# Performance work log

Hardware: AMD Instinct MI355X
Metric: run time of the kernel (lower is better)

## Reference

```python
import jax, jax.numpy as jnp
import numpy as np

NEG_SLOPE = 0.2


def _gat_layer(x, W, a_src, a_dst, b, src, dst, heads, out_dim, concat):
    # x: [N, F_in]; W: [F_in, heads*out_dim]; a_src/a_dst: [heads, out_dim]
    N = x.shape[0]
    h = (x @ W).reshape(N, heads, out_dim)              # [N, H, D]
    alpha_src = jnp.sum(h * a_src[None], axis=-1)       # [N, H]
    alpha_dst = jnp.sum(h * a_dst[None], axis=-1)       # [N, H]
    e = jax.nn.leaky_relu(alpha_src[src] + alpha_dst[dst], NEG_SLOPE)  # [E, H]
    # scatter-softmax over incoming edges of each destination node
    e_max = jax.ops.segment_max(e, dst, num_segments=N)            # [N, H]
    e_exp = jnp.exp(e - e_max[dst])                                 # [E, H]
    e_sum = jax.ops.segment_sum(e_exp, dst, num_segments=N)        # [N, H]
    alpha = e_exp / e_sum[dst]                                      # [E, H]
    # weighted scatter-sum of source features
    msg = alpha[:, :, None] * h[src]                                # [E, H, D]
    out = jax.ops.segment_sum(msg, dst, num_segments=N)             # [N, H, D]
    if concat:
        out = out.reshape(N, heads * out_dim)
    else:
        out = out.mean(axis=1)
    return out + b


def setup_inputs() -> dict:
    key = jax.random.key(0)
    ks = jax.random.split(key, 9)
    N, E, F_in, C = 100000, 1600000, 512, 40
    x = jax.random.normal(ks[0], (N, F_in), dtype=jnp.float32)
    edge_index = jax.random.randint(ks[1], (2, E), 0, N, dtype=jnp.int64)
    s = 0.05
    return {
        "x": x,
        "edge_index": edge_index,
        "W1": jax.random.normal(ks[2], (F_in, 64), dtype=jnp.float32) * s,
        "att_src1": jax.random.normal(ks[3], (8, 8), dtype=jnp.float32) * s,
        "att_dst1": jax.random.normal(ks[4], (8, 8), dtype=jnp.float32) * s,
        "b1": jnp.zeros((64,), dtype=jnp.float32),
        "W2": jax.random.normal(ks[5], (64, C), dtype=jnp.float32) * s,
        "att_src2": jax.random.normal(ks[6], (1, C), dtype=jnp.float32) * s,
        "att_dst2": jax.random.normal(ks[7], (1, C), dtype=jnp.float32) * s,
        "b2": jnp.zeros((C,), dtype=jnp.float32),
    }


def reference(x, edge_index, W1, att_src1, att_dst1, b1, W2, att_src2, att_dst2, b2):
    N = x.shape[0]
    # PyG GATConv default add_self_loops=True
    loops = jnp.tile(jnp.arange(N, dtype=edge_index.dtype)[None, :], (2, 1))
    ei = jnp.concatenate([edge_index, loops], axis=1)
    src, dst = ei[0], ei[1]
    # dropout layers are identity at inference
    h = _gat_layer(x, W1, att_src1, att_dst1, b1, src, dst, heads=8, out_dim=8, concat=True)
    h = jax.nn.elu(h)
    out = _gat_layer(h, W2, att_src2, att_dst2, b2, src, dst, heads=1, out_dim=40, concat=True)
    return jax.nn.log_softmax(out, axis=1)
```

## Files before the change

### kernel.cpp

```cpp
#include <hip/hip_runtime.h>
#include <hip/hip_bf16.h>

typedef __bf16 bf16x8 __attribute__((ext_vector_type(8)));
typedef float f32x4 __attribute__((ext_vector_type(4)));
typedef unsigned u32x2 __attribute__((ext_vector_type(2)));
typedef unsigned u32x4 __attribute__((ext_vector_type(4)));

#define LR_SLOPE 0.2f
#define NBKMAX 256
#define BCAP   12288

static __device__ __forceinline__ unsigned short f2bf(float f){
  union { float f; unsigned u; } v; v.f = f;
  unsigned u = v.u;
  u += 0x7fffu + ((u >> 16) & 1u);
  return (unsigned short)(u >> 16);
}
static __device__ __forceinline__ float bf2f(unsigned short us){
  union { unsigned u; float f; } v; v.u = ((unsigned)us) << 16;
  return v.f;
}
static __device__ __forceinline__ unsigned pk2(float a, float b){
  return (unsigned)f2bf(a) | ((unsigned)f2bf(b) << 16);
}
static __device__ __forceinline__ unsigned char f2e4m3(float f){
  return (unsigned char)(__builtin_amdgcn_cvt_pk_fp8_f32(f, 0.f, 0, false) & 0xff);
}
static __device__ __forceinline__ float e4m32f(unsigned b){
  return __builtin_amdgcn_cvt_f32_fp8(b, 0);
}
typedef float f32x4v __attribute__((ext_vector_type(4)));
static __device__ __forceinline__ f32x4v ntl4(const float* p){
  return __builtin_nontemporal_load((const f32x4v*)p);
}

__global__ void prep_w_kernel(const float* __restrict__ W1, const float* __restrict__ W2,
                              unsigned short* __restrict__ wt1, unsigned short* __restrict__ wt2,
                              int* __restrict__ bcnt){
  int t = blockIdx.x*256 + threadIdx.x;
  if (t < 512*64){
    int k = t >> 6, n = t & 63;
    wt1[n*512 + k] = f2bf(W1[t]);
  } else if (t < 512*64 + 48*64){
    int t2 = t - 512*64;
    int c = t2 >> 6, k = t2 & 63;
    wt2[t2] = (c < 40) ? f2bf(W2[k*40 + c]) : (unsigned short)0;
  } else {
    int t3 = t - (512*64 + 48*64);
    if (t3 < NBKMAX) bcnt[t3] = 0;
  }
}

__global__ __launch_bounds__(256) void gemm1_kernel(
    const float* __restrict__ x, const unsigned short* __restrict__ wt1,
    const float* __restrict__ aw_s, const float* __restrict__ aw_d,
    unsigned char* __restrict__ h1p,
    unsigned short* __restrict__ as1p, float* __restrict__ ad1, int N)
{
  __shared__ unsigned short Alds[64*72];
  const int tid = threadIdx.x;
  const int wv = tid >> 6, lane = tid & 63;
  const int c0 = lane & 15, g = lane >> 4;
  const int rowbase = blockIdx.x * 64;

  const int sr = tid >> 2, sq = tid & 3;
  const int grow = rowbase + sr;
  const bool rv = grow < N;
  const float* xp = x + (size_t)grow*512 + sq*16;
  unsigned short* wls = Alds + sr*72 + sq*16;

  f32x4 acc[4];
  acc[0] = acc[1] = acc[2] = acc[3] = (f32x4){0.f,0.f,0.f,0.f};

  const unsigned short* bp0 = wt1 + (size_t)(wv*16 + c0)*512 + g*8;

  for (int kt = 0; kt < 8; ++kt){
    f32x4v f0 = {0,0,0,0}, f1 = {0,0,0,0}, f2 = {0,0,0,0}, f3 = {0,0,0,0};
    if (rv){
      const float* p = xp + kt*64;
      f0 = ntl4(p); f1 = ntl4(p+4); f2 = ntl4(p+8); f3 = ntl4(p+12);
    }
    u32x4 w0 = { pk2(f0.x,f0.y), pk2(f0.z,f0.w), pk2(f1.x,f1.y), pk2(f1.z,f1.w) };
    u32x4 w1 = { pk2(f2.x,f2.y), pk2(f2.z,f2.w), pk2(f3.x,f3.y), pk2(f3.z,f3.w) };
    if (kt) __syncthreads();
    *(u32x4*)wls       = w0;
    *(u32x4*)(wls + 8) = w1;
    __syncthreads();
    bf16x8 b0 = *(const bf16x8*)(bp0 + kt*64);
    bf16x8 b1 = *(const bf16x8*)(bp0 + kt*64 + 32);
    #pragma unroll
    for (int mi = 0; mi < 4; ++mi){
      const unsigned short* ap = Alds + (mi*16 + c0)*72 + g*8;
      bf16x8 a0 = *(const bf16x8*)ap;
      bf16x8 a1 = *(const bf16x8*)(ap + 32);
      acc[mi] = __builtin_amdgcn_mfma_f32_16x16x32_bf16(a0, b0, acc[mi], 0,0,0);
      acc[mi] = __builtin_amdgcn_mfma_f32_16x16x32_bf16(a1, b1, acc[mi], 0,0,0);
    }
  }
  const int hh = wv*2 + (c0 >> 3);
  const float aws_l = aw_s[hh*8 + (c0 & 7)];
  const float awd_l = aw_d[hh*8 + (c0 & 7)];
  #pragma unroll
  for (int mi = 0; mi < 4; ++mi){
    #pragma unroll
    for (int i = 0; i < 4; ++i){
      int row = rowbase + mi*16 + 4*g + i;
      float av = acc[mi][i];
      if (row < N) h1p[(size_t)row*64 + wv*16 + c0] = f2e4m3(av);
      float ss = av * aws_l;
      float dd = av * awd_l;
      ss += __shfl_xor(ss, 1); ss += __shfl_xor(ss, 2); ss += __shfl_xor(ss, 4);
      dd += __shfl_xor(dd, 1); dd += __shfl_xor(dd, 2); dd += __shfl_xor(dd, 4);
      if (row < N && (c0 & 7) == 0){
        as1p[row*8 + hh] = f2bf(ss);
        ad1[row*8 + hh]  = dd;
      }
    }
  }
}

__global__ __launch_bounds__(256) void bucketA_kernel(
    const int* __restrict__ ei, int* __restrict__ bcnt,
    unsigned* __restrict__ bucketed, int E, int M, int NBK)
{
  __shared__ int hist[NBKMAX];
  __shared__ int gb[NBKMAX];
  const int tid = threadIdx.x;
  const int t0 = blockIdx.x * 2048;
  for (int i = tid; i < NBK; i += 256) hist[i] = 0;
  __syncthreads();

  unsigned pe[8]; int bk[8], rnk[8];
  #pragma unroll
  for (int j = 0; j < 8; ++j){
    int m = t0 + j*256 + tid;
    if (m < M){
      int s, d;
      if (m < E){ s = ei[m]; d = ei[E + m]; }
      else      { s = d = m - E; }
      bk[j] = d >> 9;
      pe[j] = ((unsigned)s << 9) | (unsigned)(d & 511);
      rnk[j] = atomicAdd(&hist[bk[j]], 1);
    } else bk[j] = -1;
  }
  __syncthreads();
  for (int i = tid; i < NBK; i += 256) gb[i] = atomicAdd(&bcnt[i], hist[i]);
  __syncthreads();
  #pragma unroll
  for (int j = 0; j < 8; ++j){
    if (bk[j] >= 0) bucketed[(size_t)bk[j]*BCAP + gb[bk[j]] + rnk[j]] = pe[j];
  }
}

__global__ void scanB_kernel(const int* __restrict__ bcnt, int* __restrict__ bstart,
                             int* __restrict__ rowstart, int NBK, int N, int M){
  __shared__ int sc[256];
  int t = threadIdx.x;
  int v = (t < NBK) ? bcnt[t] : 0;
  sc[t] = v; __syncthreads();
  for (int off = 1; off < 256; off <<= 1){
    int u = (t >= off) ? sc[t-off] : 0;
    __syncthreads();
    sc[t] += u;
    __syncthreads();
  }
  if (t < NBK) bstart[t] = sc[t] - v;
  if (t == 0) rowstart[N] = M;
}

__global__ __launch_bounds__(512) void bucketB_kernel(
    const unsigned* __restrict__ bucketed, const int* __restrict__ bcnt,
    const int* __restrict__ bstart,
    int* __restrict__ rowstart, int* __restrict__ csr, int N)
{
  __shared__ int cnt[512];
  __shared__ int cur[512];
  const int k = blockIdx.x;
  const int nodebase = k << 9;
  const int nn = min(512, N - nodebase);
  const int t = threadIdx.x;
  cnt[t] = 0;
  __syncthreads();
  const int ck = bcnt[k];
  const unsigned* bp = bucketed + (size_t)k*BCAP;
  for (int m = t; m < ck; m += 512) atomicAdd(&cnt[bp[m] & 511], 1);
  __syncthreads();
  int myc = cnt[t];
  cur[t] = myc; __syncthreads();
  for (int off = 1; off < 512; off <<= 1){
    int u = (t >= off) ? cur[t-off] : 0;
    __syncthreads();
    cur[t] += u;
    __syncthreads();
  }
  const int base = bstart[k];
  int excl = base + cur[t] - myc;
  if (t < nn) rowstart[nodebase + t] = excl;
  cnt[t] = excl;
  __syncthreads();
  for (int m = t; m < ck; m += 512){
    unsigned e = bp[m];
    int pos = atomicAdd(&cnt[e & 511], 1);
    csr[pos] = (int)(e >> 9);
  }
}

__global__ __launch_bounds__(256) void l1agg_kernel(
    const int* __restrict__ rowstart, const int* __restrict__ csr,
    const unsigned short* __restrict__ as1p,
    const float* __restrict__ ad1,
    const unsigned char* __restrict__ h1p,
    const float* __restrict__ b1,
    unsigned short* __restrict__ g1b, int N)
{
  int wid = blockIdx.x*4 + (threadIdx.x >> 6);
  if (wid >= N) return;
  const int lane = threadIdx.x & 63;
  const int jq  = lane >> 3;
  const int hq  = lane & 7;
  const int par = lane >> 4;
  const int q   = lane & 15;
  const int hh  = q >> 1;
  int r0 = rowstart[wid], r1 = rowstart[wid+1];
  int cnt = r1 - r0;
  int cap = cnt < 64 ? cnt : 64;
  int myidx = csr[r0 + (lane < cap ? lane : cap-1)];
  const float advq = ad1[wid*8 + hq];

  float a0 = 0.f, a1 = 0.f, a2 = 0.f, a3 = 0.f, den = 0.f;
  for (int c = 0; c < cap; c += 8){
    int se = __shfl(myidx, c + jq);
    float t = bf2f(as1p[se*8 + hq]) + advq;
    t = (t > 0.f) ? t : LR_SLOPE*t;
    float w = __expf(t);
    if (c + jq >= cap) w = 0.f;
    den += w;
    #pragma unroll
    for (int j = 0; j < 2; ++j){
      int s8 = 4*j + par;
      int sj = __shfl(myidx, c + s8);
      float wj = __shfl(w, s8*8 + hh);
      unsigned hv = *(const unsigned*)(h1p + (size_t)sj*64 + 4*q);
      a0 = fmaf(wj, __builtin_amdgcn_cvt_f32_fp8(hv, 0), a0);
      a1 = fmaf(wj, __builtin_amdgcn_cvt_f32_fp8(hv, 1), a1);
      a2 = fmaf(wj, __builtin_amdgcn_cvt_f32_fp8(hv, 2), a2);
      a3 = fmaf(wj, __builtin_amdgcn_cvt_f32_fp8(hv, 3), a3);
    }
  }
  for (int r = r0 + 64; r < r1; ++r){
    int sx = csr[r];
    float t = bf2f(as1p[sx*8 + hq]) + advq;
    t = (t > 0.f) ? t : LR_SLOPE*t;
    float w = __expf(t);
    if (lane < 8) den += w;
    float wj = __shfl(w, hh);
    if (par == 0){
      unsigned hv = *(const unsigned*)(h1p + (size_t)sx*64 + 4*q);
      a0 = fmaf(wj, __builtin_amdgcn_cvt_f32_fp8(hv, 0), a0);
      a1 = fmaf(wj, __builtin_amdgcn_cvt_f32_fp8(hv, 1), a1);
      a2 = fmaf(wj, __builtin_amdgcn_cvt_f32_fp8(hv, 2), a2);
      a3 = fmaf(wj, __builtin_amdgcn_cvt_f32_fp8(hv, 3), a3);
    }
  }
  den += __shfl_xor(den, 8); den += __shfl_xor(den, 16); den += __shfl_xor(den, 32);
  a0 += __shfl_xor(a0, 16); a0 += __shfl_xor(a0, 32);
  a1 += __shfl_xor(a1, 16); a1 += __shfl_xor(a1, 32);
  a2 += __shfl_xor(a2, 16); a2 += __shfl_xor(a2, 32);
  a3 += __shfl_xor(a3, 16); a3 += __shfl_xor(a3, 32);
  if (lane < 16){
    float rdv = 1.f / __shfl(den, hh);
    float v0 = fmaf(a0, rdv, b1[4*q]);
    float v1 = fmaf(a1, rdv, b1[4*q + 1]);
    float v2 = fmaf(a2, rdv, b1[4*q + 2]);
    float v3 = fmaf(a3, rdv, b1[4*q + 3]);
    v0 = (v0 > 0.f) ? v0 : (__expf(v0) - 1.f);
    v1 = (v1 > 0.f) ? v1 : (__expf(v1) - 1.f);
    v2 = (v2 > 0.f) ? v2 : (__expf(v2) - 1.f);
    v3 = (v3 > 0.f) ? v3 : (__expf(v3) - 1.f);
    u32x2 pk = { pk2(v0, v1), pk2(v2, v3) };
    *(u32x2*)(g1b + (size_t)wid*64 + 4*q) = pk;
  }
}

__global__ __launch_bounds__(256) void gemm2_kernel(
    const unsigned short* __restrict__ g1b, const unsigned short* __restrict__ wt2,
    const float* __restrict__ aw_s, const float* __restrict__ aw_d,
    unsigned char* __restrict__ h2p, float* __restrict__ as2, float* __restrict__ ad2, int N)
{
  __shared__ unsigned short Alds[64*72];
  const int tid = threadIdx.x;
  const int wv = tid >> 6, lane = tid & 63;
  const int c0 = lane & 15, g = lane >> 4;
  const int rowbase = blockIdx.x * 64;

  const int sr = tid >> 2, sq = tid & 3;
  const int grow = rowbase + sr;
  const bool rv = grow < N;
  u32x4 w0 = {0,0,0,0}, w1 = {0,0,0,0};
  if (rv){
    const u32x4* gp = (const u32x4*)(g1b + (size_t)grow*64 + sq*16);
    w0 = gp[0];
    w1 = gp[1];
  }
  unsigned short* wls = Alds + sr*72 + sq*16;
  *(u32x4*)wls       = w0;
  *(u32x4*)(wls + 8) = w1;
  __syncthreads();

  f32x4 acc[3];
  acc[0] = acc[1] = acc[2] = (f32x4){0.f,0.f,0.f,0.f};
  #pragma unroll
  for (int t2 = 0; t2 < 2; ++t2){
    const unsigned short* ap = Alds + (wv*16 + c0)*72 + t2*32 + g*8;
    bf16x8 a = *(const bf16x8*)ap;
    #pragma unroll
    for (int nf = 0; nf < 3; ++nf){
      bf16x8 b = *(const bf16x8*)(wt2 + (nf*16 + c0)*64 + t2*32 + g*8);
      acc[nf] = __builtin_amdgcn_mfma_f32_16x16x32_bf16(a, b, acc[nf], 0,0,0);
    }
  }
  float aws[3], awd[3];
  aws[0] = aw_s[c0];      awd[0] = aw_d[c0];
  aws[1] = aw_s[16 + c0]; awd[1] = aw_d[16 + c0];
  aws[2] = (c0 < 8) ? aw_s[32 + c0] : 0.f;
  awd[2] = (c0 < 8) ? aw_d[32 + c0] : 0.f;
  #pragma unroll
  for (int i = 0; i < 4; ++i){
    int row = rowbase + wv*16 + 4*g + i;
    float ss = 0.f, dd = 0.f;
    #pragma unroll
    for (int nf = 0; nf < 3; ++nf){
      int col = nf*16 + c0;
      float av = acc[nf][i];
      if (row < N && col < 40) h2p[(size_t)row*40 + col] = f2e4m3(av);
      float m = (col < 40) ? av : 0.f;
      ss = fmaf(m, aws[nf], ss);
      dd = fmaf(m, awd[nf], dd);
    }
    ss += __shfl_xor(ss, 1); ss += __shfl_xor(ss, 2);
    ss += __shfl_xor(ss, 4); ss += __shfl_xor(ss, 8);
    dd += __shfl_xor(dd, 1); dd += __shfl_xor(dd, 2);
    dd += __shfl_xor(dd, 4); dd += __shfl_xor(dd, 8);
    if (row < N && c0 == 0){ as2[row] = ss; ad2[row] = dd; }
  }
}

__global__ __launch_bounds__(256) void l2agg_kernel(
    const int* __restrict__ rowstart, const int* __restrict__ csr,
    const float* __restrict__ as2, const float* __restrict__ ad2,
    const unsigned char* __restrict__ h2p, const float* __restrict__ b2,
    float* __restrict__ out, int N)
{
  int wid = blockIdx.x*4 + (threadIdx.x >> 6);
  if (wid >= N) return;
  const int lane = threadIdx.x & 63;
  const int eg = lane / 10;
  const int ql = lane - eg*10;
  const bool gl = lane < 60;
  int r0 = rowstart[wid], r1 = rowstart[wid+1];
  int cnt = r1 - r0;
  int cap = cnt < 64 ? cnt : 64;
  int myidx = csr[r0 + (lane < cap ? lane : cap-1)];
  const float adv = ad2[wid];

  float t = as2[myidx] + adv;
  t = (t > 0.f) ? t : LR_SLOPE*t;
  float w = __expf(t);
  if (lane >= cap) w = 0.f;
  float den = w;
  #pragma unroll
  for (int off = 32; off; off >>= 1) den += __shfl_xor(den, off);

  float a0 = 0.f, a1 = 0.f, a2 = 0.f, a3 = 0.f;
  for (int c = 0; c < cap; c += 6){
    int slot = c + eg;
    int slc  = slot < 63 ? slot : 63;
    float wj = __shfl(w, slc);
    if (slot >= cap || !gl) wj = 0.f;
    int sj = __shfl(myidx, slc);
    if (gl){
      unsigned hv = *(const unsigned*)(h2p + (size_t)sj*40 + 4*ql);
      a0 = fmaf(wj, __builtin_amdgcn_cvt_f32_fp8(hv, 0), a0);
      a1 = fmaf(wj, __builtin_amdgcn_cvt_f32_fp8(hv, 1), a1);
      a2 = fmaf(wj, __builtin_amdgcn_cvt_f32_fp8(hv, 2), a2);
      a3 = fmaf(wj, __builtin_amdgcn_cvt_f32_fp8(hv, 3), a3);
    }
  }
  for (int r = r0 + 64; r < r1; ++r){
    int sx = csr[r];
    float tt = as2[sx] + adv;
    tt = (tt > 0.f) ? tt : LR_SLOPE*tt;
    float ww = __expf(tt);
    den += ww;
    if (eg == 0){
      unsigned hv = *(const unsigned*)(h2p + (size_t)sx*40 + 4*ql);
      a0 = fmaf(ww, __builtin_amdgcn_cvt_f32_fp8(hv, 0), a0);
      a1 = fmaf(ww, __builtin_amdgcn_cvt_f32_fp8(hv, 1), a1);
      a2 = fmaf(ww, __builtin_amdgcn_cvt_f32_fp8(hv, 2), a2);
      a3 = fmaf(ww, __builtin_amdgcn_cvt_f32_fp8(hv, 3), a3);
    }
  }
  float t0 = a0, t1 = a1, t2 = a2, t3 = a3;
  #pragma unroll
  for (int gix = 1; gix < 6; ++gix){
    int src = ((eg + gix) % 6)*10 + ql;
    t0 += __shfl(a0, src);
    t1 += __shfl(a1, src);
    t2 += __shfl(a2, src);
    t3 += __shfl(a3, src);
  }
  float rdv = 1.f/den;
  float v0 = gl ? fmaf(t0, rdv, b2[4*ql])     : -1e30f;
  float v1 = gl ? fmaf(t1, rdv, b2[4*ql + 1]) : -1e30f;
  float v2 = gl ? fmaf(t2, rdv, b2[4*ql + 2]) : -1e30f;
  float v3 = gl ? fmaf(t3, rdv, b2[4*ql + 3]) : -1e30f;
  float m = fmaxf(fmaxf(v0, v1), fmaxf(v2, v3));
  #pragma unroll
  for (int off = 32; off; off >>= 1) m = fmaxf(m, __shfl_xor(m, off));
  float sum = (eg == 0) ? (__expf(v0-m) + __expf(v1-m) + __expf(v2-m) + __expf(v3-m)) : 0.f;
  #pragma unroll
  for (int off = 32; off; off >>= 1) sum += __shfl_xor(sum, off);
  if (eg == 0){
    float ls = m + __logf(sum);
    f32x4 o = { v0 - ls, v1 - ls, v2 - ls, v3 - ls };
    *(f32x4*)(out + (size_t)wid*40 + 4*ql) = o;
  }
}

extern "C" void kernel_launch(void* const* d_in, const int* in_sizes, int n_in,
                              void* d_out, int out_size, void* d_ws, size_t ws_size,
                              hipStream_t stream)
{
  const float* x   = (const float*)d_in[0];
  const int*   ei  = (const int*)d_in[1];
  const float* W1  = (const float*)d_in[2];
  const float* aS1 = (const float*)d_in[3];
  const float* aD1 = (const float*)d_in[4];
  const float* b1  = (const float*)d_in[5];
  const float* W2  = (const float*)d_in[6];
  const float* aS2 = (const float*)d_in[7];
  const float* aD2 = (const float*)d_in[8];
  const float* b2  = (const float*)d_in[9];

  const int N   = in_sizes[0] / 512;
  const int E   = in_sizes[1] / 2;
  const int M   = E + N;
  const int NBK = (N + 511) >> 9;

  char* base = (char*)d_ws;
  size_t off = 0;
  auto alloc = [&](size_t bytes)->char* {
    char* p = base + off;
    off += (bytes + 255) & ~(size_t)255;
    return p;
  };
  unsigned char*  h1p  = (unsigned char*)alloc((size_t)N*64);
  unsigned short* g1b  = (unsigned short*)alloc((size_t)N*64*2);
  unsigned short* as1p = (unsigned short*)alloc((size_t)N*8*2);
  float* ad1      = (float*)alloc((size_t)N*8*4);
  int*   rowstart = (int*)alloc((size_t)(N+1)*4);
  int*   bcnt     = (int*)alloc((size_t)NBKMAX*4);
  int*   bstart   = (int*)alloc((size_t)NBKMAX*4);
  int*   csr      = (int*)alloc((size_t)M*4);
  unsigned* bucketed = (unsigned*)alloc((size_t)NBKMAX*BCAP*4);
  unsigned short* wt1 = (unsigned short*)alloc(64*512*2);
  unsigned short* wt2 = (unsigned short*)alloc(48*64*2);
  unsigned char* h2p = h1p;
  float* as2 = (float*)as1p;
  float* ad2 = (float*)ad1;
  float* outp = (float*)d_out;

  prep_w_kernel<<<141, 256, 0, stream>>>(W1, W2, wt1, wt2, bcnt);
  gemm1_kernel<<<(N+63)/64, 256, 0, stream>>>(x, wt1, aS1, aD1, h1p, as1p, ad1, N);
  bucketA_kernel<<<(M+2047)/2048, 256, 0, stream>>>(ei, bcnt, bucketed, E, M, NBK);
  scanB_kernel<<<1, 256, 0, stream>>>(bcnt, bstart, rowstart, NBK, N, M);
  bucketB_kernel<<<NBK, 512, 0, stream>>>(bucketed, bcnt, bstart, rowstart, csr, N);
  l1agg_kernel<<<(N+3)/4, 256, 0, stream>>>(rowstart, csr, as1p, ad1, h1p, b1, g1b, N);
  gemm2_kernel<<<(N+63)/64, 256, 0, stream>>>(g1b, wt2, aS2, aD2, h2p, as2, ad2, N);
  l2agg_kernel<<<(N+3)/4, 256, 0, stream>>>(rowstart, csr, as2, ad2, h2p, b2, outp, N);
}
```

Before: 253.5 us.

## Pack layer-2 source logit with fp8 features and fuse bucket scan

New measurement: 253.4 us. Within noise of the previous version (-0.0%).

```diff
diff --git a/kernel.cpp b/kernel.cpp
--- a/kernel.cpp
+++ b/kernel.cpp
@@ -152,35 +152,30 @@
   }
 }
 
-__global__ void scanB_kernel(const int* __restrict__ bcnt, int* __restrict__ bstart,
-                             int* __restrict__ rowstart, int NBK, int N, int M){
-  __shared__ int sc[256];
-  int t = threadIdx.x;
-  int v = (t < NBK) ? bcnt[t] : 0;
-  sc[t] = v; __syncthreads();
-  for (int off = 1; off < 256; off <<= 1){
-    int u = (t >= off) ? sc[t-off] : 0;
-    __syncthreads();
-    sc[t] += u;
-    __syncthreads();
-  }
-  if (t < NBK) bstart[t] = sc[t] - v;
-  if (t == 0) rowstart[N] = M;
-}
-
 __global__ __launch_bounds__(512) void bucketB_kernel(
     const unsigned* __restrict__ bucketed, const int* __restrict__ bcnt,
-    const int* __restrict__ bstart,
-    int* __restrict__ rowstart, int* __restrict__ csr, int N)
+    int* __restrict__ rowstart, int* __restrict__ csr, int N, int M, int NBK)
 {
   __shared__ int cnt[512];
   __shared__ int cur[512];
+  __shared__ int basevar;
   const int k = blockIdx.x;
   const int nodebase = k << 9;
   const int nn = min(512, N - nodebase);
   const int t = threadIdx.x;
+
+  cur[t] = (t < NBK) ? bcnt[t] : 0;
+  __syncthreads();
+  for (int off = 1; off < 256; off <<= 1){
+    int u = (t >= off && t < 256) ? cur[t-off] : 0;
+    __syncthreads();
+    if (t < 256) cur[t] += u;
+    __syncthreads();
+  }
+  if (t == 0) basevar = (k > 0) ? cur[k-1] : 0;
   cnt[t] = 0;
   __syncthreads();
+
   const int ck = bcnt[k];
   const unsigned* bp = bucketed + (size_t)k*BCAP;
   for (int m = t; m < ck; m += 512) atomicAdd(&cnt[bp[m] & 511], 1);
@@ -193,9 +188,10 @@
     cur[t] += u;
     __syncthreads();
   }
-  const int base = bstart[k];
+  const int base = basevar;
   int excl = base + cur[t] - myc;
   if (t < nn) rowstart[nodebase + t] = excl;
+  if (k == 0 && t == 0) rowstart[N] = M;
   cnt[t] = excl;
   __syncthreads();
   for (int m = t; m < ck; m += 512){
@@ -285,7 +281,7 @@
 __global__ __launch_bounds__(256) void gemm2_kernel(
     const unsigned short* __restrict__ g1b, const unsigned short* __restrict__ wt2,
     const float* __restrict__ aw_s, const float* __restrict__ aw_d,
-    unsigned char* __restrict__ h2p, float* __restrict__ as2, float* __restrict__ ad2, int N)
+    unsigned char* __restrict__ h2x, float* __restrict__ ad2, int N)
 {
   __shared__ unsigned short Alds[64*72];
   const int tid = threadIdx.x;
@@ -332,7 +328,7 @@
     for (int nf = 0; nf < 3; ++nf){
       int col = nf*16 + c0;
       float av = acc[nf][i];
-      if (row < N && col < 40) h2p[(size_t)row*40 + col] = f2e4m3(av);
+      if (row < N && col < 40) h2x[(size_t)row*64 + 4 + col] = f2e4m3(av);
       float m = (col < 40) ? av : 0.f;
       ss = fmaf(m, aws[nf], ss);
       dd = fmaf(m, awd[nf], dd);
@@ -341,89 +337,92 @@
     ss += __shfl_xor(ss, 4); ss += __shfl_xor(ss, 8);
     dd += __shfl_xor(dd, 1); dd += __shfl_xor(dd, 2);
     dd += __shfl_xor(dd, 4); dd += __shfl_xor(dd, 8);
-    if (row < N && c0 == 0){ as2[row] = ss; ad2[row] = dd; }
+    if (row < N && c0 == 0){
+      *(float*)(h2x + (size_t)row*64) = ss;
+      ad2[row] = dd;
+    }
   }
 }
 
 __global__ __launch_bounds__(256) void l2agg_kernel(
     const int* __restrict__ rowstart, const int* __restrict__ csr,
-    const float* __restrict__ as2, const float* __restrict__ ad2,
-    const unsigned char* __restrict__ h2p, const float* __restrict__ b2,
-    float* __restrict__ out, int N)
+    const unsigned char* __restrict__ h2x, const float* __restrict__ ad2,
+    const float* __restrict__ b2, float* __restrict__ out, int N)
 {
   int wid = blockIdx.x*4 + (threadIdx.x >> 6);
   if (wid >= N) return;
   const int lane = threadIdx.x & 63;
-  const int eg = lane / 10;
-  const int ql = lane - eg*10;
-  const bool gl = lane < 60;
+  const int eg = lane / 11;
+  const int il = lane - eg*11;
+  const bool valid = eg < 5;
   int r0 = rowstart[wid], r1 = rowstart[wid+1];
   int cnt = r1 - r0;
   int cap = cnt < 64 ? cnt : 64;
   int myidx = csr[r0 + (lane < cap ? lane : cap-1)];
   const float adv = ad2[wid];
 
-  float t = as2[myidx] + adv;
-  t = (t > 0.f) ? t : LR_SLOPE*t;
-  float w = __expf(t);
-  if (lane >= cap) w = 0.f;
-  float den = w;
-  #pragma unroll
-  for (int off = 32; off; off >>= 1) den += __shfl_xor(den, off);
-
-  float a0 = 0.f, a1 = 0.f, a2 = 0.f, a3 = 0.f;
-  for (int c = 0; c < cap; c += 6){
+  float a0 = 0.f, a1 = 0.f, a2 = 0.f, a3 = 0.f, den = 0.f;
+  for (int c = 0; c < cap; c += 5){
     int slot = c + eg;
-    int slc  = slot < 63 ? slot : 63;
-    float wj = __shfl(w, slc);
-    if (slot >= cap || !gl) wj = 0.f;
+    int slc  = slot < cap ? slot : cap-1;
     int sj = __shfl(myidx, slc);
-    if (gl){
-      unsigned hv = *(const unsigned*)(h2p + (size_t)sj*40 + 4*ql);
+    unsigned hv = valid ? *(const unsigned*)(h2x + (size_t)sj*64 + 4*il) : 0u;
+    union { unsigned u; float f; } cv; cv.u = hv;
+    float t = cv.f + adv;
+    t = (t > 0.f) ? t : LR_SLOPE*t;
+    float w = __expf(t);
+    if (slot >= cap || !valid) w = 0.f;
+    if (il == 0) den += w;
+    float wj = __shfl(w, eg*11);
+    a0 = fmaf(wj, __builtin_amdgcn_cvt_f32_fp8(hv, 0), a0);
+    a1 = fmaf(wj, __builtin_amdgcn_cvt_f32_fp8(hv, 1), a1);
+    a2 = fmaf(wj, __builtin_amdgcn_cvt_f32_fp8(hv, 2), a2);
+    a3 = fmaf(wj, __builtin_amdgcn_cvt_f32_fp8(hv, 3), a3);
+  }
+  for (int r = r0 + 64; r < r1; ++r){
+    int sx = csr[r];
+    unsigned hv = valid ? *(const unsigned*)(h2x + (size_t)sx*64 + 4*il) : 0u;
+    union { unsigned u; float f; } cv; cv.u = hv;
+    float t = cv.f + adv;
+    t = (t > 0.f) ? t : LR_SLOPE*t;
+    float w = __expf(t);
+    float wj = __shfl(w, 0);
+    if (lane == 0) den += wj;
+    if (eg == 0){
       a0 = fmaf(wj, __builtin_amdgcn_cvt_f32_fp8(hv, 0), a0);
       a1 = fmaf(wj, __builtin_amdgcn_cvt_f32_fp8(hv, 1), a1);
       a2 = fmaf(wj, __builtin_amdgcn_cvt_f32_fp8(hv, 2), a2);
       a3 = fmaf(wj, __builtin_amdgcn_cvt_f32_fp8(hv, 3), a3);
     }
   }
-  for (int r = r0 + 64; r < r1; ++r){
-    int sx = csr[r];
-    float tt = as2[sx] + adv;
-    tt = (tt > 0.f) ? tt : LR_SLOPE*tt;
-    float ww = __expf(tt);
-    den += ww;
-    if (eg == 0){
-      unsigned hv = *(const unsigned*)(h2p + (size_t)sx*40 + 4*ql);
-      a0 = fmaf(ww, __builtin_amdgcn_cvt_f32_fp8(hv, 0), a0);
-      a1 = fmaf(ww, __builtin_amdgcn_cvt_f32_fp8(hv, 1), a1);
-      a2 = fmaf(ww, __builtin_amdgcn_cvt_f32_fp8(hv, 2), a2);
-      a3 = fmaf(ww, __builtin_amdgcn_cvt_f32_fp8(hv, 3), a3);
-    }
-  }
+  #pragma unroll
+  for (int off = 32; off; off >>= 1) den += __shfl_xor(den, off);
   float t0 = a0, t1 = a1, t2 = a2, t3 = a3;
   #pragma unroll
-  for (int gix = 1; gix < 6; ++gix){
-    int src = ((eg + gix) % 6)*10 + ql;
+  for (int gix = 1; gix < 5; ++gix){
+    int src = ((eg + gix) % 5)*11 + il;
     t0 += __shfl(a0, src);
     t1 += __shfl(a1, src);
     t2 += __shfl(a2, src);
     t3 += __shfl(a3, src);
   }
+  const bool outl = (eg == 0) && (il >= 1);
+  const int fb = (il - 1)*4;
   float rdv = 1.f/den;
-  float v0 = gl ? fmaf(t0, rdv, b2[4*ql])     : -1e30f;
-  float v1 = gl ? fmaf(t1, rdv, b2[4*ql + 1]) : -1e30f;
-  float v2 = gl ? fmaf(t2, rdv, b2[4*ql + 2]) : -1e30f;
-  float v3 = gl ? fmaf(t3, rdv, b2[4*ql + 3]) : -1e30f;
+  float v0 = outl ? fmaf(t0, rdv, b2[fb])     : -1e30f;
+  float v1 = outl ? fmaf(t1, rdv, b2[fb + 1]) : -1e30f;
+  float v2 = outl ? fmaf(t2, rdv, b2[fb + 2]) : -1e30f;
+  float v3 = outl ? fmaf(t3, rdv, b2[fb + 3]) : -1e30f;
   float m = fmaxf(fmaxf(v0, v1), fmaxf(v2, v3));
   #pragma unroll
   for (int off = 32; off; off >>= 1) m = fmaxf(m, __shfl_xor(m, off));
-  float sum = (eg == 0) ? (__expf(v0-m) + __expf(v1-m) + __expf(v2-m) + __expf(v3-m)) : 0.f;
+  float sum = outl ? (__expf(v0-m) + __expf(v1-m) + __expf(v2-m) + __expf(v3-m)) : 0.f;
   #pragma unroll
   for (int off = 32; off; off >>= 1) sum += __shfl_xor(sum, off);
-  if (eg == 0){
+  if (outl){
     float ls = m + __logf(sum);
     f32x4 o = { v0 - ls, v1 - ls, v2 - ls, v3 - ls };
-    *(f32x4*)(out + (size_t)wid*40 + 4*ql) = o;
+    *(f32x4*)(out + (size_t)wid*40 + fb) = o;
   }
 }
 
@@ -460,22 +459,19 @@
   float* ad1      = (float*)alloc((size_t)N*8*4);
   int*   rowstart = (int*)alloc((size_t)(N+1)*4);
   int*   bcnt     = (int*)alloc((size_t)NBKMAX*4);
-  int*   bstart   = (int*)alloc((size_t)NBKMAX*4);
   int*   csr      = (int*)alloc((size_t)M*4);
   unsigned* bucketed = (unsigned*)alloc((size_t)NBKMAX*BCAP*4);
   unsigned short* wt1 = (unsigned short*)alloc(64*512*2);
   unsigned short* wt2 = (unsigned short*)alloc(48*64*2);
-  unsigned char* h2p = h1p;
-  float* as2 = (float*)as1p;
+  unsigned char* h2x = h1p;
   float* ad2 = (float*)ad1;
   float* outp = (float*)d_out;
 
   prep_w_kernel<<<141, 256, 0, stream>>>(W1, W2, wt1, wt2, bcnt);
   gemm1_kernel<<<(N+63)/64, 256, 0, stream>>>(x, wt1, aS1, aD1, h1p, as1p, ad1, N);
   bucketA_kernel<<<(M+2047)/2048, 256, 0, stream>>>(ei, bcnt, bucketed, E, M, NBK);
-  scanB_kernel<<<1, 256, 0, stream>>>(bcnt, bstart, rowstart, NBK, N, M);
-  bucketB_kernel<<<NBK, 512, 0, stream>>>(bucketed, bcnt, bstart, rowstart, csr, N);
+  bucketB_kernel<<<NBK, 512, 0, stream>>>(bucketed, bcnt, rowstart, csr, N, M, NBK);
   l1agg_kernel<<<(N+3)/4, 256, 0, stream>>>(rowstart, csr, as1p, ad1, h1p, b1, g1b, N);
-  gemm2_kernel<<<(N+63)/64, 256, 0, stream>>>(g1b, wt2, aS2, aD2, h2p, as2, ad2, N);
-  l2agg_kernel<<<(N+3)/4, 256, 0, stream>>>(rowstart, csr, as2, ad2, h2p, b2, outp, N);
-}
+  gemm2_kernel<<<(N+63)/64, 256, 0, stream>>>(g1b, wt2, aS2, aD2, h2x, ad2, N);
+  l2agg_kernel<<<(N+3)/4, 256, 0, stream>>>(rowstart, csr, h2x, ad2, b2, outp, N);
+}
```
